# Kernel tuning notes

Measured on AMD Instinct MI355X. Metric: run time of the kernel, lower is better.

## Reference

```python
import jax, jax.numpy as jnp
import numpy as np

N = 100000
E = 1600000
D_IN = 64
D_HID = 64
D_OUT = 64


def setup_inputs() -> dict:
    key = jax.random.key(0)
    ks = jax.random.split(key, 12)
    x = jax.random.normal(ks[0], (N, D_IN), dtype=jnp.float32)
    edge_index = jax.random.randint(ks[1], (2, E), 0, N, dtype=jnp.int64)
    s1 = 1.0 / np.sqrt(D_IN)
    s2 = 1.0 / np.sqrt(D_HID)
    return {
        "x": x,
        "edge_index": edge_index,
        "W1l": jax.random.uniform(ks[2], (D_HID, D_IN), jnp.float32, -s1, s1),
        "b1l": jax.random.uniform(ks[3], (D_HID,), jnp.float32, -s1, s1),
        "W1r": jax.random.uniform(ks[4], (D_HID, D_IN), jnp.float32, -s1, s1),
        "W2l": jax.random.uniform(ks[5], (D_HID, D_HID), jnp.float32, -s2, s2),
        "b2l": jax.random.uniform(ks[6], (D_HID,), jnp.float32, -s2, s2),
        "W2r": jax.random.uniform(ks[7], (D_HID, D_HID), jnp.float32, -s2, s2),
        "Wout": jax.random.uniform(ks[8], (D_OUT, D_HID), jnp.float32, -s2, s2),
        "bout": jax.random.uniform(ks[9], (D_OUT,), jnp.float32, -s2, s2),
        "drop": 0,
    }


def _sage_conv(x, src, dst, Wl, bl, Wr, n_nodes):
    # PyG SAGEConv, aggr='mean': out = lin_l(mean_j x_j) + lin_r(x_i)
    msg = x[src]                                            # [E, d] gather
    agg = jax.ops.segment_sum(msg, dst, num_segments=n_nodes)
    deg = jax.ops.segment_sum(jnp.ones((src.shape[0],), x.dtype), dst,
                              num_segments=n_nodes)
    mean = agg / jnp.maximum(deg, 1.0)[:, None]             # empty neighborhoods -> 0
    return mean @ Wl.T + bl + x @ Wr.T


def reference(x, edge_index, W1l, b1l, W1r, W2l, b2l, W2r, Wout, bout, drop):
    src, dst = edge_index[0], edge_index[1]
    n = x.shape[0]
    # dropout is identity in eval mode (training=False); drop unused
    h = jax.nn.relu(_sage_conv(x, src, dst, W1l, b1l, W1r, n))
    h = jax.nn.relu(_sage_conv(h, src, dst, W2l, b2l, W2r, n))
    logits = h @ Wout.T + bout
    return jax.nn.log_softmax(logits, axis=1)
```

## Files before the change

kernel.cpp:

```cpp
#include <hip/hip_runtime.h>


#define TB 256
#define TBA 1024
#define CAPB 2560

typedef __attribute__((ext_vector_type(8))) short bf16x8;
typedef __attribute__((ext_vector_type(4))) float f32x4;
typedef __attribute__((ext_vector_type(2))) float f32x2;

__device__ __forceinline__ short bf16c(float f) {
  union { float f; unsigned u; } v; v.f = f;
  unsigned r = (v.u + 0x7FFFu + ((v.u >> 16) & 1u)) >> 16;
  return (short)r;
}

__device__ __forceinline__ bf16x8 ld_bf8(const float* p) {
  float4 a = *(const float4*)p;
  float4 b = *(const float4*)(p + 4);
  bf16x8 r;
  r[0] = bf16c(a.x); r[1] = bf16c(a.y); r[2] = bf16c(a.z); r[3] = bf16c(a.w);
  r[4] = bf16c(b.x); r[5] = bf16c(b.y); r[6] = bf16c(b.z); r[7] = bf16c(b.w);
  return r;
}

__global__ void k_mode(const int* __restrict__ b, int n32, int* __restrict__ mode) {
  int lane = threadIdx.x;
  int lim = n32 < 4096 ? n32 : 4096;
  int nz = 0;
  for (int i = 2 * lane + 1; i < lim; i += 128) nz |= b[i];
  unsigned long long any = __ballot(nz != 0);
  if (lane == 0) *mode = (any == 0ull) ? 1 : 0;
}

__global__ __launch_bounds__(1024) void k_binA(
    const int* __restrict__ ei, int E, const int* __restrict__ mode,
    int* __restrict__ bucket_fill, unsigned int* __restrict__ bucketData, int NB) {
  __shared__ int hist[1024];
  __shared__ int base[1024];
  for (int i = threadIdx.x; i < NB; i += TBA) hist[i] = 0;
  __syncthreads();
  long long e0 = (long long)E * blockIdx.x / gridDim.x;
  long long e1 = (long long)E * (blockIdx.x + 1) / gridDim.x;
  bool m64 = (*mode != 0);
  for (long long e = e0 + threadIdx.x; e < e1; e += TBA) {
    int dst = m64 ? ((const int2*)ei)[(long long)E + e].x : ei[(long long)E + e];
    atomicAdd(&hist[dst >> 7], 1);
  }
  __syncthreads();
  for (int b = threadIdx.x; b < NB; b += TBA) {
    int c = hist[b];
    base[b] = c ? atomicAdd(&bucket_fill[b], c) : 0;
    hist[b] = 0;
  }
  __syncthreads();
  for (long long e = e0 + threadIdx.x; e < e1; e += TBA) {
    int src, dst;
    if (m64) {
      src = ((const int2*)ei)[e].x;
      dst = ((const int2*)ei)[(long long)E + e].x;
    } else {
      src = ei[e];
      dst = ei[(long long)E + e];
    }
    int b = dst >> 7;
    int pos = base[b] + atomicAdd(&hist[b], 1);
    if (pos < CAPB)
      bucketData[(size_t)b * CAPB + pos] =
          ((unsigned)(dst & 127) << 24) | (unsigned)src;
  }
}

__global__ __launch_bounds__(256) void k_binB(
    const unsigned int* __restrict__ bucketData, const int* __restrict__ bucket_fill,
    int* __restrict__ colp, int* __restrict__ cnt) {
  __shared__ unsigned int slice[128 * 64];
  __shared__ int lcnt[128];
  int b = blockIdx.x;
  for (int i = threadIdx.x; i < 128; i += TB) lcnt[i] = 0;
  __syncthreads();
  int fcnt = bucket_fill[b];
  if (fcnt > CAPB) fcnt = CAPB;
  const unsigned int* bd = bucketData + (size_t)b * CAPB;
  for (int k = threadIdx.x; k < fcnt; k += TB) {
    unsigned int rec = bd[k];
    int dl = rec >> 24;
    int pos = atomicAdd(&lcnt[dl], 1);
    if (pos < 64) slice[(dl << 6) + pos] = rec & 0xFFFFFFu;
  }
  __syncthreads();
  size_t obase = (size_t)b * (128 * 64);
  for (int i = threadIdx.x * 4; i < 128 * 64; i += TB * 4) {
    *(uint4*)(colp + obase + i) = *(const uint4*)(slice + i);
  }
  int node0 = b << 7;
  for (int i = threadIdx.x; i < 128; i += TB) cnt[node0 + i] = lcnt[i];
}

__global__ __launch_bounds__(256) void k_xform_mfma(
    const float* xin, const float* __restrict__ Wl, const float* __restrict__ Wr,
    const float* __restrict__ bl, unsigned short* __restrict__ y, float* zout, int n) {
  int lane = threadIdx.x & 63;
  int quad = lane >> 4, m = lane & 15;
  int w0 = (blockIdx.x * blockDim.x + threadIdx.x) >> 6;
  int nw = (gridDim.x * blockDim.x) >> 6;

  bf16x8 bfrag[8][2];
  float bias[4];
#pragma unroll
  for (int t = 0; t < 8; ++t) {
    const float* W = (t < 4) ? Wl : Wr;
    int row = (t & 3) * 16 + m;
#pragma unroll
    for (int s = 0; s < 2; ++s)
      bfrag[t][s] = ld_bf8(W + row * 64 + s * 32 + quad * 8);
  }
#pragma unroll
  for (int t = 0; t < 4; ++t) bias[t] = bl[t * 16 + m];

  int nT = (n + 15) >> 4;
  for (int tile = w0; tile < nT; tile += nw) {
    int node0 = tile << 4;
    int mrow = node0 + m;
    if (mrow >= n) mrow = n - 1;
    const float* xr = xin + (size_t)mrow * 64;
    bf16x8 a0 = ld_bf8(xr + quad * 8);
    bf16x8 a1 = ld_bf8(xr + 32 + quad * 8);

    f32x4 acc[8];
#pragma unroll
    for (int t = 0; t < 8; ++t) {
      f32x4 z4 = {0.f, 0.f, 0.f, 0.f};
      z4 = __builtin_amdgcn_mfma_f32_16x16x32_bf16(a0, bfrag[t][0], z4, 0, 0, 0);
      acc[t] = __builtin_amdgcn_mfma_f32_16x16x32_bf16(a1, bfrag[t][1], z4, 0, 0, 0);
    }

#pragma unroll
    for (int r = 0; r < 4; ++r) {
      int node = node0 + quad * 4 + r;
      if (node >= n) break;
      size_t rb = (size_t)node * 64 + m;
#pragma unroll
      for (int t = 0; t < 4; ++t)
        y[rb + t * 16] = (unsigned short)bf16c(acc[t][r]);
#pragma unroll
      for (int t = 0; t < 4; ++t)
        zout[rb + t * 16] = acc[t + 4][r] + bias[t];
    }
  }
}

__global__ __launch_bounds__(256) void k_aggr(
    const unsigned short* __restrict__ yb, const int* __restrict__ cnt,
    const int* __restrict__ colp, float* zio, int n) {
  const unsigned int* y = (const unsigned int*)yb;
  int lane = threadIdx.x & 63;
  int node = (blockIdx.x * blockDim.x + threadIdx.x) >> 6;
  if (node >= n) return;

  int deg = cnt[node];
  int jcap = deg < 64 ? deg : 64;
  int cidx = (lane < jcap) ? colp[((size_t)node << 6) + lane] : 0;

  int sub = lane >> 3;
  int fo = (lane & 7) * 4;

  f32x2 acc[4];
#pragma unroll
  for (int k = 0; k < 4; ++k) acc[k] = (f32x2){0.f, 0.f};

#define ACCUM(U)                                                              \
  do {                                                                        \
    acc[0] += (f32x2){__uint_as_float((U).x << 16),                           \
                      __uint_as_float((U).x & 0xFFFF0000u)};                  \
    acc[1] += (f32x2){__uint_as_float((U).y << 16),                           \
                      __uint_as_float((U).y & 0xFFFF0000u)};                  \
    acc[2] += (f32x2){__uint_as_float((U).z << 16),                           \
                      __uint_as_float((U).z & 0xFFFF0000u)};                  \
    acc[3] += (f32x2){__uint_as_float((U).w << 16),                           \
                      __uint_as_float((U).w & 0xFFFF0000u)};                  \
  } while (0)

  int j = 0;
  for (; j + 16 <= jcap; j += 16) {
    int ca = __shfl(cidx, j + sub, 64);
    int cb = __shfl(cidx, j + 8 + sub, 64);
    uint4 va = *(const uint4*)(y + ((size_t)ca << 5) + fo);
    uint4 vb = *(const uint4*)(y + ((size_t)cb << 5) + fo);
    ACCUM(va);
    ACCUM(vb);
  }
  for (; j < jcap; j += 8) {
    int c = __shfl(cidx, j + sub, 64);
    uint4 v = *(const uint4*)(y + ((size_t)c << 5) + fo);
    if (j + sub < jcap) ACCUM(v);
  }
#undef ACCUM

#pragma unroll
  for (int off = 8; off <= 32; off <<= 1) {
#pragma unroll
    for (int k = 0; k < 4; ++k) {
      acc[k].x += __shfl_xor(acc[k].x, off, 64);
      acc[k].y += __shfl_xor(acc[k].y, off, 64);
    }
  }

  if (lane < 8) {
    float inv = (deg > 0) ? 1.0f / (float)deg : 0.f;
    float* zp = zio + ((size_t)node << 6) + (lane * 8);
    float4 z0 = *(float4*)zp;
    float4 z1 = *(float4*)(zp + 4);
    z0.x = fmaxf(fmaf(acc[0].x, inv, z0.x), 0.f);
    z0.y = fmaxf(fmaf(acc[0].y, inv, z0.y), 0.f);
    z0.z = fmaxf(fmaf(acc[1].x, inv, z0.z), 0.f);
    z0.w = fmaxf(fmaf(acc[1].y, inv, z0.w), 0.f);
    z1.x = fmaxf(fmaf(acc[2].x, inv, z1.x), 0.f);
    z1.y = fmaxf(fmaf(acc[2].y, inv, z1.y), 0.f);
    z1.z = fmaxf(fmaf(acc[3].x, inv, z1.z), 0.f);
    z1.w = fmaxf(fmaf(acc[3].y, inv, z1.w), 0.f);
    *(float4*)zp = z0;
    *(float4*)(zp + 4) = z1;
  }
}

__global__ __launch_bounds__(256) void k_out_mfma(
    const float* __restrict__ h, const float* __restrict__ Wo,
    const float* __restrict__ bo, float* __restrict__ out, int n) {
  int lane = threadIdx.x & 63;
  int quad = lane >> 4, m = lane & 15;
  int w0 = (blockIdx.x * blockDim.x + threadIdx.x) >> 6;
  int nw = (gridDim.x * blockDim.x) >> 6;

  bf16x8 bfrag[4][2];
  float bias[4];
#pragma unroll
  for (int t = 0; t < 4; ++t) {
    int row = t * 16 + m;
#pragma unroll
    for (int s = 0; s < 2; ++s)
      bfrag[t][s] = ld_bf8(Wo + row * 64 + s * 32 + quad * 8);
    bias[t] = bo[t * 16 + m];
  }

  int nT = (n + 15) >> 4;
  for (int tile = w0; tile < nT; tile += nw) {
    int node0 = tile << 4;
    int mrow = node0 + m;
    if (mrow >= n) mrow = n - 1;
    const float* xr = h + (size_t)mrow * 64;
    bf16x8 a0 = ld_bf8(xr + quad * 8);
    bf16x8 a1 = ld_bf8(xr + 32 + quad * 8);

    f32x4 acc[4];
#pragma unroll
    for (int t = 0; t < 4; ++t) {
      f32x4 z4 = {0.f, 0.f, 0.f, 0.f};
      z4 = __builtin_amdgcn_mfma_f32_16x16x32_bf16(a0, bfrag[t][0], z4, 0, 0, 0);
      acc[t] = __builtin_amdgcn_mfma_f32_16x16x32_bf16(a1, bfrag[t][1], z4, 0, 0, 0);
    }

#pragma unroll
    for (int r = 0; r < 4; ++r) {
      int node = node0 + quad * 4 + r;
      if (node >= n) break;
      float l0 = acc[0][r] + bias[0];
      float l1 = acc[1][r] + bias[1];
      float l2 = acc[2][r] + bias[2];
      float l3 = acc[3][r] + bias[3];
      float mx = fmaxf(fmaxf(l0, l1), fmaxf(l2, l3));
#pragma unroll
      for (int off = 1; off <= 8; off <<= 1) mx = fmaxf(mx, __shfl_xor(mx, off, 64));
      float s = expf(l0 - mx) + expf(l1 - mx) + expf(l2 - mx) + expf(l3 - mx);
#pragma unroll
      for (int off = 1; off <= 8; off <<= 1) s += __shfl_xor(s, off, 64);
      float ls = logf(s);
      size_t rb = (size_t)node * 64 + m;
      out[rb + 0]  = l0 - mx - ls;
      out[rb + 16] = l1 - mx - ls;
      out[rb + 32] = l2 - mx - ls;
      out[rb + 48] = l3 - mx - ls;
    }
  }
}

extern "C" void kernel_launch(void* const* d_in, const int* in_sizes, int n_in,
                              void* d_out, int out_size, void* d_ws, size_t ws_size,
                              hipStream_t stream) {
  const float* x    = (const float*)d_in[0];
  const int*   ei   = (const int*)d_in[1];
  const float* W1l  = (const float*)d_in[2];
  const float* b1l  = (const float*)d_in[3];
  const float* W1r  = (const float*)d_in[4];
  const float* W2l  = (const float*)d_in[5];
  const float* b2l  = (const float*)d_in[6];
  const float* W2r  = (const float*)d_in[7];
  const float* Wout = (const float*)d_in[8];
  const float* bout = (const float*)d_in[9];
  int N = in_sizes[0] / 64;
  int E = in_sizes[1] / 2;
  int NB = (N + 127) >> 7;

  char* p = (char*)d_ws;
  auto carve = [&](size_t bytes) {
    char* r = p;
    p += (bytes + 255) & ~(size_t)255;
    return r;
  };
  int* mode          = (int*)carve(4);
  int* bucket_fill   = (int*)carve((size_t)NB * 4);
  int* cnt           = (int*)carve((size_t)NB * 128 * 4);
  int* colp          = (int*)carve((size_t)NB * 128 * 64 * 4);
  unsigned short* y  = (unsigned short*)carve((size_t)N * 64 * 2);
  float* z           = (float*)carve((size_t)N * 64 * 4);
  unsigned int* bucketData = (unsigned int*)z;

  hipMemsetAsync(bucket_fill, 0, (size_t)NB * 4, stream);

  k_mode<<<1, 64, 0, stream>>>(ei, 2 * E, mode);
  k_binA<<<256, TBA, 0, stream>>>(ei, E, mode, bucket_fill, bucketData, NB);
  k_binB<<<NB, TB, 0, stream>>>(bucketData, bucket_fill, colp, cnt);

  int aggr_blocks = (N + 3) / 4;
  k_xform_mfma<<<512, TB, 0, stream>>>(x, W1l, W1r, b1l, y, z, N);
  k_aggr<<<aggr_blocks, TB, 0, stream>>>(y, cnt, colp, z, N);
  k_xform_mfma<<<512, TB, 0, stream>>>(z, W2l, W2r, b2l, y, z, N);
  k_aggr<<<aggr_blocks, TB, 0, stream>>>(y, cnt, colp, z, N);
  k_out_mfma<<<512, TB, 0, stream>>>(z, Wout, bout, (float*)d_out, N);
}
```

Before: 265.1 us.

## Pack four nodes per wavefront in aggregation and fold int64 mode detection into binning

The aggregation kernel now gives each node 16 lanes and packs four nodes into one wavefront. Each node still gathers 8 features per lane from two neighbour slots per step, with loops bounded by the maximum degree in the wave. This targets wasted lanes and long serial loops when the average degree is around 16, at the cost of divergence when degrees within a wave differ. The separate mode-detection kernel launch is also removed: each binning block checks the int64 layout of the edge index redundantly itself.

```diff
diff --git a/kernel.cpp b/kernel.cpp
--- a/kernel.cpp
+++ b/kernel.cpp
@@ -24,25 +24,23 @@
   return r;
 }
 
-__global__ void k_mode(const int* __restrict__ b, int n32, int* __restrict__ mode) {
-  int lane = threadIdx.x;
-  int lim = n32 < 4096 ? n32 : 4096;
-  int nz = 0;
-  for (int i = 2 * lane + 1; i < lim; i += 128) nz |= b[i];
-  unsigned long long any = __ballot(nz != 0);
-  if (lane == 0) *mode = (any == 0ull) ? 1 : 0;
-}
-
 __global__ __launch_bounds__(1024) void k_binA(
-    const int* __restrict__ ei, int E, const int* __restrict__ mode,
+    const int* __restrict__ ei, int E,
     int* __restrict__ bucket_fill, unsigned int* __restrict__ bucketData, int NB) {
   __shared__ int hist[1024];
   __shared__ int base[1024];
+  __shared__ int s_nz;
+  if (threadIdx.x == 0) s_nz = 0;
   for (int i = threadIdx.x; i < NB; i += TBA) hist[i] = 0;
   __syncthreads();
+  int nz = 0;
+  for (int i = threadIdx.x; i < 2048; i += TBA) nz |= ei[2 * i + 1];
+  if (nz) atomicOr(&s_nz, 1);
+  __syncthreads();
+  bool m64 = (s_nz == 0);
+
   long long e0 = (long long)E * blockIdx.x / gridDim.x;
   long long e1 = (long long)E * (blockIdx.x + 1) / gridDim.x;
-  bool m64 = (*mode != 0);
   for (long long e = e0 + threadIdx.x; e < e1; e += TBA) {
     int dst = m64 ? ((const int2*)ei)[(long long)E + e].x : ei[(long long)E + e];
     atomicAdd(&hist[dst >> 7], 1);
@@ -155,15 +153,24 @@
     const int* __restrict__ colp, float* zio, int n) {
   const unsigned int* y = (const unsigned int*)yb;
   int lane = threadIdx.x & 63;
-  int node = (blockIdx.x * blockDim.x + threadIdx.x) >> 6;
-  if (node >= n) return;
-
-  int deg = cnt[node];
+  int wv = (blockIdx.x * blockDim.x + threadIdx.x) >> 6;
+  int g16 = lane & 48;
+  int lig = lane & 15;
+  int sub = lig >> 3;
+  int fo = (lig & 7) * 4;
+
+  int node = (wv << 2) + (g16 >> 4);
+  bool act = node < n;
+  int cn = act ? node : 0;
+  int deg = cnt[cn];
   int jcap = deg < 64 ? deg : 64;
-  int cidx = (lane < jcap) ? colp[((size_t)node << 6) + lane] : 0;
-
-  int sub = lane >> 3;
-  int fo = (lane & 7) * 4;
+  size_t crow = (size_t)cn << 6;
+  int cidxA = colp[crow + lig];
+  int cidxB = colp[crow + 16 + lig];
+
+  int wmax = jcap;
+  wmax = max(wmax, __shfl_xor(wmax, 16, 64));
+  wmax = max(wmax, __shfl_xor(wmax, 32, 64));
 
   f32x2 acc[4];
 #pragma unroll
@@ -175,40 +182,71 @@
                       __uint_as_float((U).x & 0xFFFF0000u)};                  \
     acc[1] += (f32x2){__uint_as_float((U).y << 16),                           \
                       __uint_as_float((U).y & 0xFFFF0000u)};                  \
-    acc[2] += (f32x2){__uint_as_float((U).z << 16),                           \
+    acc[2] += (f32x2){__uint_as_float((U).z << 16),                          \
                       __uint_as_float((U).z & 0xFFFF0000u)};                  \
     acc[3] += (f32x2){__uint_as_float((U).w << 16),                           \
                       __uint_as_float((U).w & 0xFFFF0000u)};                  \
   } while (0)
 
-  int j = 0;
-  for (; j + 16 <= jcap; j += 16) {
-    int ca = __shfl(cidx, j + sub, 64);
-    int cb = __shfl(cidx, j + 8 + sub, 64);
-    uint4 va = *(const uint4*)(y + ((size_t)ca << 5) + fo);
-    uint4 vb = *(const uint4*)(y + ((size_t)cb << 5) + fo);
-    ACCUM(va);
-    ACCUM(vb);
-  }
-  for (; j < jcap; j += 8) {
-    int c = __shfl(cidx, j + sub, 64);
-    uint4 v = *(const uint4*)(y + ((size_t)c << 5) + fo);
-    if (j + sub < jcap) ACCUM(v);
+  {
+    int lim = wmax < 16 ? wmax : 16;
+    for (int s = 0; s < lim; s += 2) {
+      int slot = s + sub;
+      int c = __shfl(cidxA, g16 | slot, 64);
+      if (slot < jcap) {
+        uint4 v = *(const uint4*)(y + ((size_t)c << 5) + fo);
+        ACCUM(v);
+      }
+    }
+  }
+  if (wmax > 16) {
+    int lim = (wmax < 32 ? wmax : 32) - 16;
+    for (int s = 0; s < lim; s += 2) {
+      int slot = s + sub;
+      int c = __shfl(cidxB, g16 | slot, 64);
+      if (slot + 16 < jcap) {
+        uint4 v = *(const uint4*)(y + ((size_t)c << 5) + fo);
+        ACCUM(v);
+      }
+    }
+  }
+  if (wmax > 32) {
+    int cidxC = colp[crow + 32 + lig];
+    int cidxD = colp[crow + 48 + lig];
+    {
+      int lim = (wmax < 48 ? wmax : 48) - 32;
+      for (int s = 0; s < lim; s += 2) {
+        int slot = s + sub;
+        int c = __shfl(cidxC, g16 | slot, 64);
+        if (slot + 32 < jcap) {
+          uint4 v = *(const uint4*)(y + ((size_t)c << 5) + fo);
+          ACCUM(v);
+        }
+      }
+    }
+    if (wmax > 48) {
+      int lim = wmax - 48;
+      for (int s = 0; s < lim; s += 2) {
+        int slot = s + sub;
+        int c = __shfl(cidxD, g16 | slot, 64);
+        if (slot + 48 < jcap) {
+          uint4 v = *(const uint4*)(y + ((size_t)c << 5) + fo);
+          ACCUM(v);
+        }
+      }
+    }
   }
 #undef ACCUM
 
 #pragma unroll
-  for (int off = 8; off <= 32; off <<= 1) {
-#pragma unroll
-    for (int k = 0; k < 4; ++k) {
-      acc[k].x += __shfl_xor(acc[k].x, off, 64);
-      acc[k].y += __shfl_xor(acc[k].y, off, 64);
-    }
-  }
-
-  if (lane < 8) {
+  for (int k = 0; k < 4; ++k) {
+    acc[k].x += __shfl_xor(acc[k].x, 8, 64);
+    acc[k].y += __shfl_xor(acc[k].y, 8, 64);
+  }
+
+  if (act && sub == 0) {
     float inv = (deg > 0) ? 1.0f / (float)deg : 0.f;
-    float* zp = zio + ((size_t)node << 6) + (lane * 8);
+    float* zp = zio + ((size_t)node << 6) + fo * 2;
     float4 z0 = *(float4*)zp;
     float4 z1 = *(float4*)(zp + 4);
     z0.x = fmaxf(fmaf(acc[0].x, inv, z0.x), 0.f);
@@ -307,7 +345,6 @@
     p += (bytes + 255) & ~(size_t)255;
     return r;
   };
-  int* mode          = (int*)carve(4);
   int* bucket_fill   = (int*)carve((size_t)NB * 4);
   int* cnt           = (int*)carve((size_t)NB * 128 * 4);
   int* colp          = (int*)carve((size_t)NB * 128 * 64 * 4);
@@ -317,11 +354,10 @@
 
   hipMemsetAsync(bucket_fill, 0, (size_t)NB * 4, stream);
 
-  k_mode<<<1, 64, 0, stream>>>(ei, 2 * E, mode);
-  k_binA<<<256, TBA, 0, stream>>>(ei, E, mode, bucket_fill, bucketData, NB);
+  k_binA<<<256, TBA, 0, stream>>>(ei, E, bucket_fill, bucketData, NB);
   k_binB<<<NB, TB, 0, stream>>>(bucketData, bucket_fill, colp, cnt);
 
-  int aggr_blocks = (N + 3) / 4;
+  int aggr_blocks = (N + 15) / 16;
   k_xform_mfma<<<512, TB, 0, stream>>>(x, W1l, W1r, b1l, y, z, N);
   k_aggr<<<aggr_blocks, TB, 0, stream>>>(y, cnt, colp, z, N);
   k_xform_mfma<<<512, TB, 0, stream>>>(z, W2l, W2r, b2l, y, z, N);
```

Measured after the change: 250.6 us. 5.5% less time.
